# Kernel tuning notes

Hardware: AMD Instinct MI355X
Metric: run time of the kernel (lower is better)

Reference implementation:

```python
import jax, jax.numpy as jnp
import numpy as np

H = 1024   # hidden_dim
F = 4096   # ffn_dim
E = 8      # n_experts
K = 2      # topk
B, S = 2, 1024


def setup_inputs() -> dict:
    key = jax.random.key(0)
    k0, k1, k2, k3, k4 = jax.random.split(key, 5)
    s = 0.02
    x = jax.random.normal(k0, (B, S, H), dtype=jnp.float32)
    Wr = jax.random.normal(k1, (E, H), dtype=jnp.float32) * s      # router Linear weight [E,H]
    W1 = jax.random.normal(k2, (E, H, F), dtype=jnp.float32) * s   # expert gate proj
    W3 = jax.random.normal(k3, (E, H, F), dtype=jnp.float32) * s   # expert up proj
    W2 = jax.random.normal(k4, (E, F, H), dtype=jnp.float32) * s   # expert down proj
    return {"x": x, "Wr": Wr, "W1": W1, "W2": W2, "W3": W3}


def reference(x, Wr, W1, W2, W3):
    b, s, h = x.shape
    xf = x.reshape(-1, h)                      # [T, H]
    T = xf.shape[0]
    # --- router ---
    logits = xf @ Wr.T                         # [T, E]
    probs = jax.nn.softmax(logits, axis=-1)
    _, idx = jax.lax.top_k(probs, K)           # [T, K] expert indices
    w = jnp.take_along_axis(probs, idx, axis=-1)
    w = w / w.sum(axis=-1, keepdims=True)      # renormalize selected weights
    # dense combine matrix [T, E]: zero for unselected experts
    combine = jnp.zeros((T, E), xf.dtype).at[jnp.arange(T)[:, None], idx].set(w)
    # --- experts (SwiGLU FFN, evaluated densely then masked by combine) ---
    gate = jax.nn.silu(jnp.einsum('th,ehf->tef', xf, W1))
    up = jnp.einsum('th,ehf->tef', xf, W3)
    hmid = gate * up                            # [T, E, F]
    out = jnp.einsum('te,tef,efh->th', combine, hmid, W2)
    return out.reshape(b, s, h)
```

## Files before the change

kernel.cpp:

```cpp
#include <hip/hip_runtime.h>
#include <hip/hip_bf16.h>
#include <math.h>

#define HD 1024
#define FD 4096
#define NE 8
#define NT 2048
#define BM 128
#define BN 128
#define BK 32

#define WS_LISTS   1024
#define WS_ROUTEW  (1024 + NE*NT*4)
#define WS_XB      ((size_t)1 << 20)
#define WS_HMID    ((size_t)8 << 20)
#define WS_WBUF    ((size_t)48 << 20)
#define WS_OPAIR   ((size_t)112 << 20)

typedef __attribute__((ext_vector_type(8))) short bf16x8;
typedef __attribute__((ext_vector_type(4))) float f32x4;

static __device__ __forceinline__ unsigned int pk_bf16(float a, float b) {
    __hip_bfloat162 h = __float22bfloat162_rn(make_float2(a, b));
    return *reinterpret_cast<unsigned int*>(&h);
}

static __device__ __forceinline__ void gll16(const void* g, void* l) {
    __builtin_amdgcn_global_load_lds(
        (const __attribute__((address_space(1))) unsigned int*)g,
        (__attribute__((address_space(3))) unsigned int*)l,
        16, 0, 0);
}

__global__ void prep_kernel(const float* __restrict__ x, unsigned short* __restrict__ xb,
                            int* __restrict__ counts) {
    int idx = blockIdx.x * 256 + threadIdx.x;
    if (idx < NE) counts[idx] = 0;
    float4 v = *(const float4*)(x + (size_t)idx * 4);
    *(uint2*)(xb + (size_t)idx * 4) = make_uint2(pk_bf16(v.x, v.y), pk_bf16(v.z, v.w));
}

__global__ __launch_bounds__(128)
void router_kernel(const float* __restrict__ x, const float* __restrict__ Wr,
                   int* __restrict__ counts, int* __restrict__ lists,
                   float* __restrict__ route_w) {
    int t = blockIdx.x;
    int tid = threadIdx.x;
    float acc[NE];
#pragma unroll
    for (int e = 0; e < NE; e++) acc[e] = 0.f;
    const float* xt = x + (size_t)t * HD;
    for (int h = tid; h < HD; h += 128) {
        float xv = xt[h];
#pragma unroll
        for (int e = 0; e < NE; e++) acc[e] += xv * Wr[e * HD + h];
    }
    __shared__ float red[NE][128];
#pragma unroll
    for (int e = 0; e < NE; e++) red[e][tid] = acc[e];
    __syncthreads();
    for (int s = 64; s > 0; s >>= 1) {
        if (tid < s) {
#pragma unroll
            for (int e = 0; e < NE; e++) red[e][tid] += red[e][tid + s];
        }
        __syncthreads();
    }
    if (tid == 0) {
        int i0 = 0; float l0 = red[0][0];
        for (int e = 1; e < NE; e++) { float v = red[e][0]; if (v > l0) { l0 = v; i0 = e; } }
        int i1 = -1; float l1 = -3.0e38f;
        for (int e = 0; e < NE; e++) {
            if (e == i0) continue;
            float v = red[e][0]; if (v > l1) { l1 = v; i1 = e; }
        }
        float w0 = 1.f / (1.f + expf(l1 - l0));
        float w1 = 1.f - w0;
        int s0 = atomicAdd(&counts[i0], 1);
        lists[i0 * NT + s0] = t * 2;
        route_w[t * 2] = w0;
        int s1 = atomicAdd(&counts[i1], 1);
        lists[i1 * NT + s1] = t * 2 + 1;
        route_w[t * 2 + 1] = w1;
    }
}

__global__ __launch_bounds__(256)
void transp_kernel(const float* __restrict__ srcA, const float* __restrict__ srcB,
                   unsigned short* __restrict__ dst, int R, int C) {
    __shared__ float tile[64][65];
    int z = blockIdx.z;
    const float* src = (z < 8) ? (srcA + (size_t)z * R * C) : (srcB + (size_t)(z - 8) * R * C);
    unsigned short* d = dst + (size_t)z * R * C;
    int c0 = blockIdx.x * 64, r0 = blockIdx.y * 64;
    int t = threadIdx.x;
    int rr = t >> 4, cc = (t & 15) * 4;
#pragma unroll
    for (int i = 0; i < 4; i++) {
        int r = rr + i * 16;
        float4 v = *(const float4*)(src + (size_t)(r0 + r) * C + c0 + cc);
        tile[cc + 0][r] = v.x; tile[cc + 1][r] = v.y;
        tile[cc + 2][r] = v.z; tile[cc + 3][r] = v.w;
    }
    __syncthreads();
    int cl = t >> 2, rc = (t & 3) * 16;
    unsigned int o[8];
#pragma unroll
    for (int i = 0; i < 8; i++)
        o[i] = pk_bf16(tile[cl][rc + 2 * i], tile[cl][rc + 2 * i + 1]);
    unsigned short* dp = d + (size_t)(c0 + cl) * R + r0 + rc;
    *(uint4*)(dp)     = make_uint4(o[0], o[1], o[2], o[3]);
    *(uint4*)(dp + 8) = make_uint4(o[4], o[5], o[6], o[7]);
}

__global__ __launch_bounds__(256, 2)
void gemm1_kernel(const unsigned short* __restrict__ xb, const unsigned short* __restrict__ wbuf,
                  const int* __restrict__ counts, const int* __restrict__ lists,
                  unsigned short* __restrict__ hmid) {
    int xcd = blockIdx.x;
    int y = blockIdx.y;
    int en = xcd + 8 * (y >> 4);
    int mblk = y & 15;
    int e = en >> 5;
    int nblk = en & 31;
    int cnt = counts[e];
    int m0 = mblk * BM;
    if (m0 >= cnt) return;
    int n0 = nblk * BN;
    const unsigned short* W1b = wbuf + (size_t)e * FD * HD;
    const unsigned short* W3b = wbuf + (size_t)(8 + e) * FD * HD;

    __shared__ __align__(16) unsigned short As[128 * 32];
    __shared__ __align__(16) unsigned short B1s[128 * 32];
    __shared__ __align__(16) unsigned short B3s[128 * 32];
    __shared__ int rp_s[128];

    int tid = threadIdx.x;
    if (tid < 128) {
        int m = m0 + tid;
        rp_s[tid] = (m < cnt) ? lists[e * NT + m] : lists[e * NT];
    }
    __syncthreads();

    const int w = tid >> 6;
    const int lane = tid & 63;
    const int srow = lane >> 2;
    const int schunk = lane & 3;

    const unsigned short *gA[2], *gB1[2], *gB3[2];
    unsigned short *lA[2], *lB1[2], *lB3[2];
#pragma unroll
    for (int q = 0; q < 2; q++) {
        int row = w * 32 + q * 16 + srow;
        gA[q]  = xb  + (size_t)(rp_s[row] >> 1) * HD + schunk * 8;
        gB1[q] = W1b + (size_t)(n0 + row) * HD + schunk * 8;
        gB3[q] = W3b + (size_t)(n0 + row) * HD + schunk * 8;
        lA[q]  = &As [(w * 32 + q * 16) * 32];
        lB1[q] = &B1s[(w * 32 + q * 16) * 32];
        lB3[q] = &B3s[(w * 32 + q * 16) * 32];
    }

    const int wr = w >> 1, wc = w & 1;
    const int lm = lane & 15, lg = lane >> 4;

    f32x4 zf = {0.f, 0.f, 0.f, 0.f};
    f32x4 accG[4][4], accU[4][4];
#pragma unroll
    for (int i = 0; i < 4; i++)
#pragma unroll
        for (int j = 0; j < 4; j++) { accG[i][j] = zf; accU[i][j] = zf; }

    for (int h0 = 0; h0 < HD; h0 += BK) {
        __syncthreads();
#pragma unroll
        for (int q = 0; q < 2; q++) {
            gll16(gA[q] + h0, lA[q]);
            gll16(gB1[q] + h0, lB1[q]);
            gll16(gB3[q] + h0, lB3[q]);
        }
        __syncthreads();

        bf16x8 af[4], b1f[4], b3f[4];
#pragma unroll
        for (int i = 0; i < 4; i++)
            af[i] = *(const bf16x8*)&As[(wr * 64 + i * 16 + lm) * 32 + lg * 8];
#pragma unroll
        for (int j = 0; j < 4; j++) {
            b1f[j] = *(const bf16x8*)&B1s[(wc * 64 + j * 16 + lm) * 32 + lg * 8];
            b3f[j] = *(const bf16x8*)&B3s[(wc * 64 + j * 16 + lm) * 32 + lg * 8];
        }
#pragma unroll
        for (int i = 0; i < 4; i++)
#pragma unroll
            for (int j = 0; j < 4; j++) {
                accG[i][j] = __builtin_amdgcn_mfma_f32_16x16x32_bf16(af[i], b1f[j], accG[i][j], 0, 0, 0);
                accU[i][j] = __builtin_amdgcn_mfma_f32_16x16x32_bf16(af[i], b3f[j], accU[i][j], 0, 0, 0);
            }
    }

#pragma unroll
    for (int i = 0; i < 4; i++) {
#pragma unroll
        for (int r = 0; r < 4; r++) {
            int ml = wr * 64 + i * 16 + lg * 4 + r;
            int m = m0 + ml;
            if (m < cnt) {
                int p = rp_s[ml];
                unsigned short* hrow = hmid + (size_t)p * FD + n0 + wc * 64 + lm;
#pragma unroll
                for (int j = 0; j < 4; j++) {
                    float g = accG[i][j][r];
                    float u = accU[i][j][r];
                    float v = (g / (1.f + expf(-g))) * u;
                    __hip_bfloat16 hb = __float2bfloat16(v);
                    hrow[j * 16] = *reinterpret_cast<unsigned short*>(&hb);
                }
            }
        }
    }
}

__global__ __launch_bounds__(256, 2)
void gemm2_kernel(const unsigned short* __restrict__ hmid, const unsigned short* __restrict__ wbuf,
                  const int* __restrict__ counts, const int* __restrict__ lists,
                  float* __restrict__ opair) {
    int xcd = blockIdx.x;
    int y = blockIdx.y;
    int grp = xcd + 8 * (y >> 4);
    int mblk = y & 15;
    int ks = grp >> 6;
    int rest = grp & 63;
    int e = rest >> 3;
    int nblk = rest & 7;
    int cnt = counts[e];
    int m0 = mblk * BM;
    if (m0 >= cnt) return;
    int n0 = nblk * BN;
    const unsigned short* W2b = wbuf + (size_t)e * HD * FD;

    __shared__ __align__(16) unsigned short As[128 * 32];
    __shared__ __align__(16) unsigned short Bs[128 * 32];
    __shared__ int rp_s[128];

    int tid = threadIdx.x;
    if (tid < 128) {
        int m = m0 + tid;
        rp_s[tid] = (m < cnt) ? lists[e * NT + m] : lists[e * NT];
    }
    __syncthreads();

    const int w = tid >> 6;
    const int lane = tid & 63;
    const int srow = lane >> 2;
    const int schunk = lane & 3;

    const unsigned short *gA[2], *gB[2];
    unsigned short *lA[2], *lB[2];
#pragma unroll
    for (int q = 0; q < 2; q++) {
        int row = w * 32 + q * 16 + srow;
        gA[q] = hmid + (size_t)rp_s[row] * FD + schunk * 8;
        gB[q] = W2b + (size_t)(n0 + row) * FD + schunk * 8;
        lA[q] = &As[(w * 32 + q * 16) * 32];
        lB[q] = &Bs[(w * 32 + q * 16) * 32];
    }

    const int wr = w >> 1, wc = w & 1;
    const int lm = lane & 15, lg = lane >> 4;

    f32x4 zf = {0.f, 0.f, 0.f, 0.f};
    f32x4 acc[4][4];
#pragma unroll
    for (int i = 0; i < 4; i++)
#pragma unroll
        for (int j = 0; j < 4; j++) acc[i][j] = zf;

    const int f_begin = ks * (FD / 2);
    const int f_end = f_begin + FD / 2;
    for (int f0 = f_begin; f0 < f_end; f0 += BK) {
        __syncthreads();
#pragma unroll
        for (int q = 0; q < 2; q++) {
            gll16(gA[q] + f0, lA[q]);
            gll16(gB[q] + f0, lB[q]);
        }
        __syncthreads();

        bf16x8 af[4], bf[4];
#pragma unroll
        for (int i = 0; i < 4; i++)
            af[i] = *(const bf16x8*)&As[(wr * 64 + i * 16 + lm) * 32 + lg * 8];
#pragma unroll
        for (int j = 0; j < 4; j++)
            bf[j] = *(const bf16x8*)&Bs[(wc * 64 + j * 16 + lm) * 32 + lg * 8];
#pragma unroll
        for (int i = 0; i < 4; i++)
#pragma unroll
            for (int j = 0; j < 4; j++)
                acc[i][j] = __builtin_amdgcn_mfma_f32_16x16x32_bf16(af[i], bf[j], acc[i][j], 0, 0, 0);
    }

#pragma unroll
    for (int i = 0; i < 4; i++) {
#pragma unroll
        for (int r = 0; r < 4; r++) {
            int ml = wr * 64 + i * 16 + lg * 4 + r;
            int m = m0 + ml;
            if (m < cnt) {
                int p = rp_s[ml];
                float* op = opair + ((size_t)ks * (2 * NT) + p) * HD + n0 + wc * 64 + lm;
#pragma unroll
                for (int j = 0; j < 4; j++) op[j * 16] = acc[i][j][r];
            }
        }
    }
}

__global__ __launch_bounds__(256)
void combine_kernel(const float* __restrict__ opair, const float* __restrict__ route_w,
                    float* __restrict__ out) {
    int idx = blockIdx.x * 256 + threadIdx.x;
    int tok = idx >> 8;
    int hc = (idx & 255) * 4;
    const float* o0 = opair;
    const float* o1 = opair + (size_t)(2 * NT) * HD;
    size_t r0 = (size_t)(2 * tok) * HD + hc;
    size_t r1 = (size_t)(2 * tok + 1) * HD + hc;
    float w0 = route_w[2 * tok], w1 = route_w[2 * tok + 1];
    float4 a = *(const float4*)(o0 + r0);
    float4 b = *(const float4*)(o1 + r0);
    float4 c = *(const float4*)(o0 + r1);
    float4 d = *(const float4*)(o1 + r1);
    float4 r;
    r.x = w0 * (a.x + b.x) + w1 * (c.x + d.x);
    r.y = w0 * (a.y + b.y) + w1 * (c.y + d.y);
    r.z = w0 * (a.z + b.z) + w1 * (c.z + d.z);
    r.w = w0 * (a.w + b.w) + w1 * (c.w + d.w);
    *(float4*)(out + (size_t)tok * HD + hc) = r;
}

extern "C" void kernel_launch(void* const* d_in, const int* in_sizes, int n_in,
                              void* d_out, int out_size, void* d_ws, size_t ws_size,
                              hipStream_t stream) {
    const float* x  = (const float*)d_in[0];
    const float* Wr = (const float*)d_in[1];
    const float* W1 = (const float*)d_in[2];
    const float* W2 = (const float*)d_in[3];
    const float* W3 = (const float*)d_in[4];
    float* out = (float*)d_out;

    char* ws = (char*)d_ws;
    int*   counts  = (int*)(ws);
    int*   lists   = (int*)(ws + WS_LISTS);
    float* route_w = (float*)(ws + WS_ROUTEW);
    unsigned short* xb   = (unsigned short*)(ws + WS_XB);
    unsigned short* hmid = (unsigned short*)(ws + WS_HMID);
    unsigned short* wbuf = (unsigned short*)(ws + WS_WBUF);
    float* opair = (float*)(ws + WS_OPAIR);

    hipLaunchKernelGGL(prep_kernel, dim3(2048), dim3(256), 0, stream, x, xb, counts);
    hipLaunchKernelGGL(router_kernel, dim3(NT), dim3(128), 0, stream,
                       x, Wr, counts, lists, route_w);
    hipLaunchKernelGGL(transp_kernel, dim3(FD / 64, HD / 64, 16), dim3(256), 0, stream,
                       W1, W3, wbuf, HD, FD);
    hipLaunchKernelGGL(gemm1_kernel, dim3(8, 512), dim3(256), 0, stream,
                       xb, wbuf, counts, lists, hmid);
    hipLaunchKernelGGL(transp_kernel, dim3(HD / 64, FD / 64, 8), dim3(256), 0, stream,
                       W2, W2, wbuf, FD, HD);
    hipLaunchKernelGGL(gemm2_kernel, dim3(8, 256), dim3(256), 0, stream,
                       hmid, wbuf, counts, lists, opair);
    hipLaunchKernelGGL(combine_kernel, dim3(2048), dim3(256), 0, stream,
                       opair, route_w, out);
}
```

Measured before the change: 666.6 us.

## Fuse fp32 weight transpose/convert into GEMM loaders with register prefetch

Drops the separate transpose kernels that turned W1/W3/W2 into bf16 transposed buffers. Each GEMM now reads fp32 weights straight from global memory into registers, prefetched one K-step ahead, then packs them to bf16 and writes them into padded shared-memory tiles. The aim is to avoid writing and re-reading the full converted weight copies and to cut two kernel launches. In exchange, every M-block re-reads and re-converts fp32 weights, which doubles B-operand global traffic per tile and raises register pressure.

```diff
diff --git a/kernel.cpp b/kernel.cpp
--- a/kernel.cpp
+++ b/kernel.cpp
@@ -14,8 +14,7 @@
 #define WS_ROUTEW  (1024 + NE*NT*4)
 #define WS_XB      ((size_t)1 << 20)
 #define WS_HMID    ((size_t)8 << 20)
-#define WS_WBUF    ((size_t)48 << 20)
-#define WS_OPAIR   ((size_t)112 << 20)
+#define WS_OPAIR   ((size_t)48 << 20)
 
 typedef __attribute__((ext_vector_type(8))) short bf16x8;
 typedef __attribute__((ext_vector_type(4))) float f32x4;
@@ -85,36 +84,22 @@
     }
 }
 
-__global__ __launch_bounds__(256)
-void transp_kernel(const float* __restrict__ srcA, const float* __restrict__ srcB,
-                   unsigned short* __restrict__ dst, int R, int C) {
-    __shared__ float tile[64][65];
-    int z = blockIdx.z;
-    const float* src = (z < 8) ? (srcA + (size_t)z * R * C) : (srcB + (size_t)(z - 8) * R * C);
-    unsigned short* d = dst + (size_t)z * R * C;
-    int c0 = blockIdx.x * 64, r0 = blockIdx.y * 64;
-    int t = threadIdx.x;
-    int rr = t >> 4, cc = (t & 15) * 4;
-#pragma unroll
-    for (int i = 0; i < 4; i++) {
-        int r = rr + i * 16;
-        float4 v = *(const float4*)(src + (size_t)(r0 + r) * C + c0 + cc);
-        tile[cc + 0][r] = v.x; tile[cc + 1][r] = v.y;
-        tile[cc + 2][r] = v.z; tile[cc + 3][r] = v.w;
-    }
-    __syncthreads();
-    int cl = t >> 2, rc = (t & 3) * 16;
-    unsigned int o[8];
-#pragma unroll
-    for (int i = 0; i < 8; i++)
-        o[i] = pk_bf16(tile[cl][rc + 2 * i], tile[cl][rc + 2 * i + 1]);
-    unsigned short* dp = d + (size_t)(c0 + cl) * R + r0 + rc;
-    *(uint4*)(dp)     = make_uint4(o[0], o[1], o[2], o[3]);
-    *(uint4*)(dp + 8) = make_uint4(o[4], o[5], o[6], o[7]);
-}
+#define LOADB_PAIR(buf, base, stride, h)  do {                                   \
+    const float* _p = (base) + (size_t)(h) * (stride);                           \
+    buf[0] = *(const float4*)(_p);          buf[1] = *(const float4*)(_p + (stride)); \
+    buf[2] = *(const float4*)(_p + 64);     buf[3] = *(const float4*)(_p + (stride) + 64); \
+} while (0)
+
+#define PK4(udst, noff, va, vb)  do {                                            \
+    udst[((noff) + 0) * 20 + kpr] = pk_bf16(va.x, vb.x);                         \
+    udst[((noff) + 1) * 20 + kpr] = pk_bf16(va.y, vb.y);                         \
+    udst[((noff) + 2) * 20 + kpr] = pk_bf16(va.z, vb.z);                         \
+    udst[((noff) + 3) * 20 + kpr] = pk_bf16(va.w, vb.w);                         \
+} while (0)
 
 __global__ __launch_bounds__(256, 2)
-void gemm1_kernel(const unsigned short* __restrict__ xb, const unsigned short* __restrict__ wbuf,
+void gemm1_kernel(const unsigned short* __restrict__ xb, const float* __restrict__ W1,
+                  const float* __restrict__ W3,
                   const int* __restrict__ counts, const int* __restrict__ lists,
                   unsigned short* __restrict__ hmid) {
     int xcd = blockIdx.x;
@@ -127,12 +112,12 @@
     int m0 = mblk * BM;
     if (m0 >= cnt) return;
     int n0 = nblk * BN;
-    const unsigned short* W1b = wbuf + (size_t)e * FD * HD;
-    const unsigned short* W3b = wbuf + (size_t)(8 + e) * FD * HD;
+    const float* W1e = W1 + (size_t)e * HD * FD;
+    const float* W3e = W3 + (size_t)e * HD * FD;
 
     __shared__ __align__(16) unsigned short As[128 * 32];
-    __shared__ __align__(16) unsigned short B1s[128 * 32];
-    __shared__ __align__(16) unsigned short B3s[128 * 32];
+    __shared__ __align__(16) unsigned short B1s[128 * 40];
+    __shared__ __align__(16) unsigned short B3s[128 * 40];
     __shared__ int rp_s[128];
 
     int tid = threadIdx.x;
@@ -147,18 +132,22 @@
     const int srow = lane >> 2;
     const int schunk = lane & 3;
 
-    const unsigned short *gA[2], *gB1[2], *gB3[2];
-    unsigned short *lA[2], *lB1[2], *lB3[2];
+    const unsigned short* gA[2];
+    unsigned short* lA[2];
 #pragma unroll
     for (int q = 0; q < 2; q++) {
         int row = w * 32 + q * 16 + srow;
-        gA[q]  = xb  + (size_t)(rp_s[row] >> 1) * HD + schunk * 8;
-        gB1[q] = W1b + (size_t)(n0 + row) * HD + schunk * 8;
-        gB3[q] = W3b + (size_t)(n0 + row) * HD + schunk * 8;
-        lA[q]  = &As [(w * 32 + q * 16) * 32];
-        lB1[q] = &B1s[(w * 32 + q * 16) * 32];
-        lB3[q] = &B3s[(w * 32 + q * 16) * 32];
-    }
+        gA[q] = xb + (size_t)(rp_s[row] >> 1) * HD + schunk * 8;
+        lA[q] = &As[(w * 32 + q * 16) * 32];
+    }
+
+    const int kp  = (tid & 15) * 2;
+    const int kpr = tid & 15;
+    const int nqa = tid >> 4;
+    const float* pB1 = W1e + (size_t)kp * FD + n0 + nqa * 4;
+    const float* pB3 = W3e + (size_t)kp * FD + n0 + nqa * 4;
+    unsigned int* uB1 = (unsigned int*)B1s;
+    unsigned int* uB3 = (unsigned int*)B3s;
 
     const int wr = w >> 1, wc = w & 1;
     const int lm = lane & 15, lg = lane >> 4;
@@ -170,33 +159,47 @@
 #pragma unroll
         for (int j = 0; j < 4; j++) { accG[i][j] = zf; accU[i][j] = zf; }
 
-    for (int h0 = 0; h0 < HD; h0 += BK) {
-        __syncthreads();
-#pragma unroll
-        for (int q = 0; q < 2; q++) {
-            gll16(gA[q] + h0, lA[q]);
-            gll16(gB1[q] + h0, lB1[q]);
-            gll16(gB3[q] + h0, lB3[q]);
-        }
-        __syncthreads();
-
-        bf16x8 af[4], b1f[4], b3f[4];
-#pragma unroll
-        for (int i = 0; i < 4; i++)
-            af[i] = *(const bf16x8*)&As[(wr * 64 + i * 16 + lm) * 32 + lg * 8];
-#pragma unroll
-        for (int j = 0; j < 4; j++) {
-            b1f[j] = *(const bf16x8*)&B1s[(wc * 64 + j * 16 + lm) * 32 + lg * 8];
-            b3f[j] = *(const bf16x8*)&B3s[(wc * 64 + j * 16 + lm) * 32 + lg * 8];
-        }
-#pragma unroll
-        for (int i = 0; i < 4; i++)
-#pragma unroll
-            for (int j = 0; j < 4; j++) {
-                accG[i][j] = __builtin_amdgcn_mfma_f32_16x16x32_bf16(af[i], b1f[j], accG[i][j], 0, 0, 0);
-                accU[i][j] = __builtin_amdgcn_mfma_f32_16x16x32_bf16(af[i], b3f[j], accU[i][j], 0, 0, 0);
-            }
-    }
+    float4 bufA[8], bufB[8];
+    LOADB_PAIR(bufA,       pB1, FD, 0);
+    LOADB_PAIR((bufA + 4), pB3, FD, 0);
+
+#define G1_STEP(CUR, NXT, H0)  do {                                              \
+    __syncthreads();                                   \
+    gll16(gA[0] + (H0), lA[0]); gll16(gA[1] + (H0), lA[1]);                      \
+    if ((H0) + BK < HD) {                                                        \
+        LOADB_PAIR(NXT,       pB1, FD, (H0) + BK);                               \
+        LOADB_PAIR((NXT + 4), pB3, FD, (H0) + BK);                               \
+    }                                                                            \
+    PK4(uB1, nqa * 4,        CUR[0], CUR[1]);                                    \
+    PK4(uB1, (nqa + 16) * 4, CUR[2], CUR[3]);                                    \
+    PK4(uB3, nqa * 4,        CUR[4], CUR[5]);                                    \
+    PK4(uB3, (nqa + 16) * 4, CUR[6], CUR[7]);                                    \
+    __syncthreads();                                       \
+    {                                                                            \
+        bf16x8 af[4], b1f[4], b3f[4];                                            \
+        _Pragma("unroll")                                                        \
+        for (int i = 0; i < 4; i++)                                              \
+            af[i] = *(const bf16x8*)&As[(wr * 64 + i * 16 + lm) * 32 + lg * 8];  \
+        _Pragma("unroll")                                                        \
+        for (int j = 0; j < 4; j++) {                                            \
+            b1f[j] = *(const bf16x8*)&B1s[(wc * 64 + j * 16 + lm) * 40 + lg * 8];\
+            b3f[j] = *(const bf16x8*)&B3s[(wc * 64 + j * 16 + lm) * 40 + lg * 8];\
+        }                                                                        \
+        _Pragma("unroll")                                                        \
+        for (int i = 0; i < 4; i++)                                              \
+            _Pragma("unroll")                                                    \
+            for (int j = 0; j < 4; j++) {                                        \
+                accG[i][j] = __builtin_amdgcn_mfma_f32_16x16x32_bf16(af[i], b1f[j], accG[i][j], 0, 0, 0); \
+                accU[i][j] = __builtin_amdgcn_mfma_f32_16x16x32_bf16(af[i], b3f[j], accU[i][j], 0, 0, 0); \
+            }                                                                    \
+    }                                                                            \
+} while (0)
+
+    for (int h0 = 0; h0 < HD; h0 += 2 * BK) {
+        G1_STEP(bufA, bufB, h0);
+        G1_STEP(bufB, bufA, h0 + BK);
+    }
+#undef G1_STEP
 
 #pragma unroll
     for (int i = 0; i < 4; i++) {
@@ -221,7 +224,7 @@
 }
 
 __global__ __launch_bounds__(256, 2)
-void gemm2_kernel(const unsigned short* __restrict__ hmid, const unsigned short* __restrict__ wbuf,
+void gemm2_kernel(const unsigned short* __restrict__ hmid, const float* __restrict__ W2,
                   const int* __restrict__ counts, const int* __restrict__ lists,
                   float* __restrict__ opair) {
     int xcd = blockIdx.x;
@@ -236,10 +239,10 @@
     int m0 = mblk * BM;
     if (m0 >= cnt) return;
     int n0 = nblk * BN;
-    const unsigned short* W2b = wbuf + (size_t)e * HD * FD;
+    const float* W2e = W2 + (size_t)e * FD * HD;
 
     __shared__ __align__(16) unsigned short As[128 * 32];
-    __shared__ __align__(16) unsigned short Bs[128 * 32];
+    __shared__ __align__(16) unsigned short Bs[128 * 40];
     __shared__ int rp_s[128];
 
     int tid = threadIdx.x;
@@ -254,16 +257,20 @@
     const int srow = lane >> 2;
     const int schunk = lane & 3;
 
-    const unsigned short *gA[2], *gB[2];
-    unsigned short *lA[2], *lB[2];
+    const unsigned short* gA[2];
+    unsigned short* lA[2];
 #pragma unroll
     for (int q = 0; q < 2; q++) {
         int row = w * 32 + q * 16 + srow;
         gA[q] = hmid + (size_t)rp_s[row] * FD + schunk * 8;
-        gB[q] = W2b + (size_t)(n0 + row) * FD + schunk * 8;
         lA[q] = &As[(w * 32 + q * 16) * 32];
-        lB[q] = &Bs[(w * 32 + q * 16) * 32];
-    }
+    }
+
+    const int kp  = (tid & 15) * 2;
+    const int kpr = tid & 15;
+    const int nqa = tid >> 4;
+    const float* pB2 = W2e + (size_t)kp * HD + n0 + nqa * 4;
+    unsigned int* uB = (unsigned int*)Bs;
 
     const int wr = w >> 1, wc = w & 1;
     const int lm = lane & 15, lg = lane >> 4;
@@ -276,29 +283,39 @@
         for (int j = 0; j < 4; j++) acc[i][j] = zf;
 
     const int f_begin = ks * (FD / 2);
-    const int f_end = f_begin + FD / 2;
-    for (int f0 = f_begin; f0 < f_end; f0 += BK) {
-        __syncthreads();
-#pragma unroll
-        for (int q = 0; q < 2; q++) {
-            gll16(gA[q] + f0, lA[q]);
-            gll16(gB[q] + f0, lB[q]);
-        }
-        __syncthreads();
-
-        bf16x8 af[4], bf[4];
-#pragma unroll
-        for (int i = 0; i < 4; i++)
-            af[i] = *(const bf16x8*)&As[(wr * 64 + i * 16 + lm) * 32 + lg * 8];
-#pragma unroll
-        for (int j = 0; j < 4; j++)
-            bf[j] = *(const bf16x8*)&Bs[(wc * 64 + j * 16 + lm) * 32 + lg * 8];
-#pragma unroll
-        for (int i = 0; i < 4; i++)
-#pragma unroll
-            for (int j = 0; j < 4; j++)
-                acc[i][j] = __builtin_amdgcn_mfma_f32_16x16x32_bf16(af[i], bf[j], acc[i][j], 0, 0, 0);
-    }
+    const int f_end   = f_begin + FD / 2;
+
+    float4 bufA[4], bufB[4];
+    LOADB_PAIR(bufA, pB2, HD, f_begin);
+
+#define G2_STEP(CUR, NXT, F0)  do {                                              \
+    __syncthreads();                                                             \
+    gll16(gA[0] + (F0), lA[0]); gll16(gA[1] + (F0), lA[1]);                      \
+    if ((F0) + BK < f_end) { LOADB_PAIR(NXT, pB2, HD, (F0) + BK); }              \
+    PK4(uB, nqa * 4,        CUR[0], CUR[1]);                                     \
+    PK4(uB, (nqa + 16) * 4, CUR[2], CUR[3]);                                     \
+    __syncthreads();                                                             \
+    {                                                                            \
+        bf16x8 af[4], bf[4];                                                     \
+        _Pragma("unroll")                                                        \
+        for (int i = 0; i < 4; i++)                                              \
+            af[i] = *(const bf16x8*)&As[(wr * 64 + i * 16 + lm) * 32 + lg * 8];  \
+        _Pragma("unroll")                                                        \
+        for (int j = 0; j < 4; j++)                                              \
+            bf[j] = *(const bf16x8*)&Bs[(wc * 64 + j * 16 + lm) * 40 + lg * 8];  \
+        _Pragma("unroll")                                                        \
+        for (int i = 0; i < 4; i++)                                              \
+            _Pragma("unroll")                                                    \
+            for (int j = 0; j < 4; j++)                                          \
+                acc[i][j] = __builtin_amdgcn_mfma_f32_16x16x32_bf16(af[i], bf[j], acc[i][j], 0, 0, 0); \
+    }                                                                            \
+} while (0)
+
+    for (int f0 = f_begin; f0 < f_end; f0 += 2 * BK) {
+        G2_STEP(bufA, bufB, f0);
+        G2_STEP(bufB, bufA, f0 + BK);
+    }
+#undef G2_STEP
 
 #pragma unroll
     for (int i = 0; i < 4; i++) {
@@ -355,20 +372,15 @@
     float* route_w = (float*)(ws + WS_ROUTEW);
     unsigned short* xb   = (unsigned short*)(ws + WS_XB);
     unsigned short* hmid = (unsigned short*)(ws + WS_HMID);
-    unsigned short* wbuf = (unsigned short*)(ws + WS_WBUF);
     float* opair = (float*)(ws + WS_OPAIR);
 
     hipLaunchKernelGGL(prep_kernel, dim3(2048), dim3(256), 0, stream, x, xb, counts);
     hipLaunchKernelGGL(router_kernel, dim3(NT), dim3(128), 0, stream,
                        x, Wr, counts, lists, route_w);
-    hipLaunchKernelGGL(transp_kernel, dim3(FD / 64, HD / 64, 16), dim3(256), 0, stream,
-                       W1, W3, wbuf, HD, FD);
     hipLaunchKernelGGL(gemm1_kernel, dim3(8, 512), dim3(256), 0, stream,
-                       xb, wbuf, counts, lists, hmid);
-    hipLaunchKernelGGL(transp_kernel, dim3(HD / 64, FD / 64, 8), dim3(256), 0, stream,
-                       W2, W2, wbuf, FD, HD);
+                       xb, W1, W3, counts, lists, hmid);
     hipLaunchKernelGGL(gemm2_kernel, dim3(8, 256), dim3(256), 0, stream,
-                       hmid, wbuf, counts, lists, opair);
+                       hmid, W2, counts, lists, opair);
     hipLaunchKernelGGL(combine_kernel, dim3(2048), dim3(256), 0, stream,
                        opair, route_w, out);
 }
```

After: 713.9 us. 1.07x slower.

## Compact expert tile work list, swizzle LDS layout, raise occupancy hint

Applied to the files above, without the earlier changes.

A small plan kernel builds a compact list of (expert, m-block) tiles from the routing counts, so the two grouped GEMMs launch only valid tiles instead of a padded grid with early-exit blocks. The grid order also changes so that all N-tiles of one expert/m-block are consecutive in x, which changes L2 reuse patterns compared with the previous XCD-aware mapping. LDS tiles are XOR-swizzled per row pair to reduce bank conflicts on the bf16x8 fragment reads, and launch_bounds min blocks goes from 2 to 4. The single-thread plan kernel adds a serial launch, and the occupancy hint may force register spills given the large accumulator sets in gemm1.

```diff
diff --git a/kernel.cpp b/kernel.cpp
--- a/kernel.cpp
+++ b/kernel.cpp
@@ -12,6 +12,7 @@
 
 #define WS_LISTS   1024
 #define WS_ROUTEW  (1024 + NE*NT*4)
+#define WS_WORK    (WS_ROUTEW + NT*2*4)
 #define WS_XB      ((size_t)1 << 20)
 #define WS_HMID    ((size_t)8 << 20)
 #define WS_WBUF    ((size_t)48 << 20)
@@ -82,6 +83,17 @@
         int s1 = atomicAdd(&counts[i1], 1);
         lists[i1 * NT + s1] = t * 2 + 1;
         route_w[t * 2 + 1] = w1;
+    }
+}
+
+__global__ void plan_kernel(const int* __restrict__ counts, int* __restrict__ work) {
+    if (threadIdx.x == 0) {
+        int c = 0;
+        for (int e = 0; e < NE; e++) {
+            int cnt = counts[e];
+            for (int m0 = 0; m0 < cnt; m0 += BM) work[c++] = (e << 20) | m0;
+        }
+        for (int i = c; i < 64; i++) work[i] = -1;
     }
 }
 
@@ -113,20 +125,16 @@
     *(uint4*)(dp + 8) = make_uint4(o[4], o[5], o[6], o[7]);
 }
 
-__global__ __launch_bounds__(256, 2)
+__global__ __launch_bounds__(256, 4)
 void gemm1_kernel(const unsigned short* __restrict__ xb, const unsigned short* __restrict__ wbuf,
                   const int* __restrict__ counts, const int* __restrict__ lists,
-                  unsigned short* __restrict__ hmid) {
-    int xcd = blockIdx.x;
-    int y = blockIdx.y;
-    int en = xcd + 8 * (y >> 4);
-    int mblk = y & 15;
-    int e = en >> 5;
-    int nblk = en & 31;
+                  const int* __restrict__ work, unsigned short* __restrict__ hmid) {
+    int wi = work[blockIdx.y];
+    if (wi < 0) return;
+    int e = wi >> 20;
+    int m0 = wi & 0xFFFFF;
     int cnt = counts[e];
-    int m0 = mblk * BM;
-    if (m0 >= cnt) return;
-    int n0 = nblk * BN;
+    int n0 = blockIdx.x * BN;
     const unsigned short* W1b = wbuf + (size_t)e * FD * HD;
     const unsigned short* W3b = wbuf + (size_t)(8 + e) * FD * HD;
 
@@ -152,9 +160,10 @@
 #pragma unroll
     for (int q = 0; q < 2; q++) {
         int row = w * 32 + q * 16 + srow;
-        gA[q]  = xb  + (size_t)(rp_s[row] >> 1) * HD + schunk * 8;
-        gB1[q] = W1b + (size_t)(n0 + row) * HD + schunk * 8;
-        gB3[q] = W3b + (size_t)(n0 + row) * HD + schunk * 8;
+        int sc = schunk ^ ((row >> 1) & 3);
+        gA[q]  = xb  + (size_t)(rp_s[row] >> 1) * HD + sc * 8;
+        gB1[q] = W1b + (size_t)(n0 + row) * HD + sc * 8;
+        gB3[q] = W3b + (size_t)(n0 + row) * HD + sc * 8;
         lA[q]  = &As [(w * 32 + q * 16) * 32];
         lB1[q] = &B1s[(w * 32 + q * 16) * 32];
         lB3[q] = &B3s[(w * 32 + q * 16) * 32];
@@ -162,6 +171,15 @@
 
     const int wr = w >> 1, wc = w & 1;
     const int lm = lane & 15, lg = lane >> 4;
+
+    int aoff[4], boff[4];
+#pragma unroll
+    for (int i = 0; i < 4; i++) {
+        int ra = wr * 64 + i * 16 + lm;
+        aoff[i] = ra * 32 + (lg ^ ((ra >> 1) & 3)) * 8;
+        int rb = wc * 64 + i * 16 + lm;
+        boff[i] = rb * 32 + (lg ^ ((rb >> 1) & 3)) * 8;
+    }
 
     f32x4 zf = {0.f, 0.f, 0.f, 0.f};
     f32x4 accG[4][4], accU[4][4];
@@ -183,11 +201,11 @@
         bf16x8 af[4], b1f[4], b3f[4];
 #pragma unroll
         for (int i = 0; i < 4; i++)
-            af[i] = *(const bf16x8*)&As[(wr * 64 + i * 16 + lm) * 32 + lg * 8];
+            af[i] = *(const bf16x8*)&As[aoff[i]];
 #pragma unroll
         for (int j = 0; j < 4; j++) {
-            b1f[j] = *(const bf16x8*)&B1s[(wc * 64 + j * 16 + lm) * 32 + lg * 8];
-            b3f[j] = *(const bf16x8*)&B3s[(wc * 64 + j * 16 + lm) * 32 + lg * 8];
+            b1f[j] = *(const bf16x8*)&B1s[boff[j]];
+            b3f[j] = *(const bf16x8*)&B3s[boff[j]];
         }
 #pragma unroll
         for (int i = 0; i < 4; i++)
@@ -220,22 +238,18 @@
     }
 }
 
-__global__ __launch_bounds__(256, 2)
+__global__ __launch_bounds__(256, 4)
 void gemm2_kernel(const unsigned short* __restrict__ hmid, const unsigned short* __restrict__ wbuf,
                   const int* __restrict__ counts, const int* __restrict__ lists,
-                  float* __restrict__ opair) {
-    int xcd = blockIdx.x;
-    int y = blockIdx.y;
-    int grp = xcd + 8 * (y >> 4);
-    int mblk = y & 15;
-    int ks = grp >> 6;
-    int rest = grp & 63;
-    int e = rest >> 3;
-    int nblk = rest & 7;
+                  const int* __restrict__ work, float* __restrict__ opair) {
+    int yy = blockIdx.y;
+    int ks = yy >> 6;
+    int wi = work[yy & 63];
+    if (wi < 0) return;
+    int e = wi >> 20;
+    int m0 = wi & 0xFFFFF;
     int cnt = counts[e];
-    int m0 = mblk * BM;
-    if (m0 >= cnt) return;
-    int n0 = nblk * BN;
+    int n0 = blockIdx.x * BN;
     const unsigned short* W2b = wbuf + (size_t)e * HD * FD;
 
     __shared__ __align__(16) unsigned short As[128 * 32];
@@ -259,14 +273,24 @@
 #pragma unroll
     for (int q = 0; q < 2; q++) {
         int row = w * 32 + q * 16 + srow;
-        gA[q] = hmid + (size_t)rp_s[row] * FD + schunk * 8;
-        gB[q] = W2b + (size_t)(n0 + row) * FD + schunk * 8;
+        int sc = schunk ^ ((row >> 1) & 3);
+        gA[q] = hmid + (size_t)rp_s[row] * FD + sc * 8;
+        gB[q] = W2b + (size_t)(n0 + row) * FD + sc * 8;
         lA[q] = &As[(w * 32 + q * 16) * 32];
         lB[q] = &Bs[(w * 32 + q * 16) * 32];
     }
 
     const int wr = w >> 1, wc = w & 1;
     const int lm = lane & 15, lg = lane >> 4;
+
+    int aoff[4], boff[4];
+#pragma unroll
+    for (int i = 0; i < 4; i++) {
+        int ra = wr * 64 + i * 16 + lm;
+        aoff[i] = ra * 32 + (lg ^ ((ra >> 1) & 3)) * 8;
+        int rb = wc * 64 + i * 16 + lm;
+        boff[i] = rb * 32 + (lg ^ ((rb >> 1) & 3)) * 8;
+    }
 
     f32x4 zf = {0.f, 0.f, 0.f, 0.f};
     f32x4 acc[4][4];
@@ -289,10 +313,10 @@
         bf16x8 af[4], bf[4];
 #pragma unroll
         for (int i = 0; i < 4; i++)
-            af[i] = *(const bf16x8*)&As[(wr * 64 + i * 16 + lm) * 32 + lg * 8];
+            af[i] = *(const bf16x8*)&As[aoff[i]];
 #pragma unroll
         for (int j = 0; j < 4; j++)
-            bf[j] = *(const bf16x8*)&Bs[(wc * 64 + j * 16 + lm) * 32 + lg * 8];
+            bf[j] = *(const bf16x8*)&Bs[boff[j]];
 #pragma unroll
         for (int i = 0; i < 4; i++)
 #pragma unroll
@@ -353,6 +377,7 @@
     int*   counts  = (int*)(ws);
     int*   lists   = (int*)(ws + WS_LISTS);
     float* route_w = (float*)(ws + WS_ROUTEW);
+    int*   work    = (int*)(ws + WS_WORK);
     unsigned short* xb   = (unsigned short*)(ws + WS_XB);
     unsigned short* hmid = (unsigned short*)(ws + WS_HMID);
     unsigned short* wbuf = (unsigned short*)(ws + WS_WBUF);
@@ -361,14 +386,15 @@
     hipLaunchKernelGGL(prep_kernel, dim3(2048), dim3(256), 0, stream, x, xb, counts);
     hipLaunchKernelGGL(router_kernel, dim3(NT), dim3(128), 0, stream,
                        x, Wr, counts, lists, route_w);
+    hipLaunchKernelGGL(plan_kernel, dim3(1), dim3(64), 0, stream, counts, work);
     hipLaunchKernelGGL(transp_kernel, dim3(FD / 64, HD / 64, 16), dim3(256), 0, stream,
                        W1, W3, wbuf, HD, FD);
-    hipLaunchKernelGGL(gemm1_kernel, dim3(8, 512), dim3(256), 0, stream,
-                       xb, wbuf, counts, lists, hmid);
+    hipLaunchKernelGGL(gemm1_kernel, dim3(FD / BN, 64), dim3(256), 0, stream,
+                       xb, wbuf, counts, lists, work, hmid);
     hipLaunchKernelGGL(transp_kernel, dim3(HD / 64, FD / 64, 8), dim3(256), 0, stream,
                        W2, W2, wbuf, FD, HD);
-    hipLaunchKernelGGL(gemm2_kernel, dim3(8, 256), dim3(256), 0, stream,
-                       hmid, wbuf, counts, lists, opair);
+    hipLaunchKernelGGL(gemm2_kernel, dim3(HD / BN, 128), dim3(256), 0, stream,
+                       hmid, wbuf, counts, lists, work, opair);
     hipLaunchKernelGGL(combine_kernel, dim3(2048), dim3(256), 0, stream,
                        opair, route_w, out);
 }
```

New measurement: 1.524 ms. 2.29x slower.
